# Performance work log

Hardware: AMD Instinct MI355X
Metric: run time of the kernel (lower is better)

Reference implementation:

```python
import jax, jax.numpy as jnp
import numpy as np


def _lga_pass(x, filters, radius):
    # x: [N, C, H, W]; filters: [N, (2r+1)^2, H, W]
    # out[n,c,h,w] = sum_{i,j in [-r,r]} filters[n,(i+r)*(2r+1)+(j+r),h,w] * x[n,c,h+i,w+j]
    N, C, H, W = x.shape
    k = 2 * radius + 1
    xp = jnp.pad(x, ((0, 0), (0, 0), (radius, radius), (radius, radius)))
    out = jnp.zeros_like(x)
    idx = 0
    for i in range(k):  # fixed small kernel loop (25 taps), accumulates without materializing [N,C,H,W,25]
        for j in range(k):
            out = out + filters[:, idx:idx + 1] * xp[:, :, i:i + H, j:j + W]
            idx += 1
    return out


def setup_inputs() -> dict:
    key = jax.random.key(0)
    k1, k2 = jax.random.split(key)
    input1 = jax.random.normal(k1, (2, 64, 256, 512), dtype=jnp.float32)
    input2 = jax.random.uniform(k2, (2, 25, 256, 512), dtype=jnp.float32)
    return {"input1": input1, "input2": input2, "radius": 2}


def reference(input1, input2, radius):
    # LGA applied twice with the same per-pixel filters (Lga2Function.forward)
    temp = _lga_pass(input1, input2, radius)
    out = _lga_pass(temp, input2, radius)
    return out
```

## Files before the change

kernel.cpp:

```cpp
#include <hip/hip_runtime.h>
#include <hip/hip_fp16.h>


typedef __fp16 h2v __attribute__((ext_vector_type(2)));

#define OH 12
#define OW 60
#define USH 40

__device__ __forceinline__ unsigned pkh(float a, float b) {
    union { h2v h; unsigned u; } c;
    c.h = __builtin_amdgcn_cvt_pkrtz(a, b);
    return c.u;
}

#define PKF(ac, fv, xv) \
    asm("v_pk_fma_f16 %0, %1, %2, %0" : "+v"(ac) : "v"(fv), "v"(xv));

#define ROWP(i, w0, w1, w2, w3, D01, D23) { \
    const unsigned A01 = ((w0) >> 16) | ((w1) << 16); \
    const unsigned A12 = ((w1) >> 16) | ((w2) << 16); \
    const unsigned A23 = ((w2) >> 16) | ((w3) << 16); \
    PKF(D01, frA[5*(i)+0], w0)  PKF(D01, frA[5*(i)+1], A01) \
    PKF(D01, frA[5*(i)+2], w1)  PKF(D01, frA[5*(i)+3], A12) \
    PKF(D01, frA[5*(i)+4], w2) \
    PKF(D23, frB[5*(i)+0], w1)  PKF(D23, frB[5*(i)+1], A12) \
    PKF(D23, frB[5*(i)+2], w2)  PKF(D23, frB[5*(i)+3], A23) \
    PKF(D23, frB[5*(i)+4], w3) }

#define PASSP(BUF, ROWBASE) { \
    unsigned e01 = 0u, o01 = 0u, e23 = 0u, o23 = 0u; \
    _Pragma("unroll") \
    for (int i = 0; i < 5; ++i) { \
        const int b = ((ROWBASE) + i) * USH + 2 * s; \
        uint2 lo = *(const uint2*)&(BUF)[b]; \
        uint2 hi = *(const uint2*)&(BUF)[b + 2]; \
        if (i & 1) { ROWP(i, lo.x, lo.y, hi.x, hi.y, o01, o23) } \
        else       { ROWP(i, lo.x, lo.y, hi.x, hi.y, e01, e23) } \
    } \
    asm("v_pk_add_f16 %0, %1, %2" : "=v"(s01) : "v"(e01), "v"(o01)); \
    asm("v_pk_add_f16 %0, %1, %2" : "=v"(s23) : "v"(e23), "v"(o23)); }

#define LBAR() { asm volatile("s_waitcnt lgkmcnt(0)" ::: "memory"); \
                 __builtin_amdgcn_s_barrier(); asm volatile("" ::: "memory"); }

__global__ __launch_bounds__(256)
void lga2_fused(const float* __restrict__ x, const float* __restrict__ f,
                float* __restrict__ out, int N, int C, int H, int W, int CPB) {
    const int tid = threadIdx.x;
    const int r = tid >> 4;
    const int s = tid & 15;
    const int oh0 = blockIdx.y * OH;
    const int ow0 = blockIdx.x * OW;
    const int CG = C / CPB;
    const int n  = blockIdx.z / CG;
    const int c0 = (blockIdx.z % CG) * CPB;
    const int HW = H * W;

    __shared__ unsigned sxU[2][20 * USH];
    __shared__ unsigned stU[16 * USH];

    if (tid < 32) {
        int row = tid & 15;
        stU[row * USH + ((tid & 16) ? 33 : 0)] = 0u;
    }

    const int gh_f = oh0 - 2 + r;
    const int gwb  = ow0 - 2 + 4 * s;
    const bool rowok = (gh_f >= 0) && (gh_f < H);
    const bool p0ok = rowok && (gwb >= 0) && (gwb + 1 < W);
    const bool p1ok = rowok && (gwb + 3 < W);
    const float* fb = f + (size_t)(n * 25) * HW + (size_t)(rowok ? gh_f : 0) * W;

    unsigned frA[25], frB[25];
    #pragma unroll
    for (int t = 0; t < 25; ++t) {
        float2 v01 = p0ok ? *(const float2*)(fb + (size_t)t * HW + gwb)
                          : make_float2(0.f, 0.f);
        float2 v23 = p1ok ? *(const float2*)(fb + (size_t)t * HW + gwb + 2)
                          : make_float2(0.f, 0.f);
        frA[t] = pkh(v01.x, v01.y);
        frB[t] = pkh(v23.x, v23.y);
        if (t == 12) __builtin_amdgcn_sched_barrier(0);
    }
    #pragma unroll
    for (int t = 0; t < 25; ++t)
        asm volatile("" : "+v"(frA[t]), "+v"(frB[t]));

    const int i1 = tid + 256;
    const bool has1 = (tid < 340 - 256);
    const int row0 = tid / 17, v0 = tid - row0 * 17;
    const int row1 = i1 / 17,  v1 = i1 - row1 * 17;
    const int g0h = oh0 - 4 + row0, g0c = ow0 - 4 + 4 * v0;
    const int g1h = oh0 - 4 + row1, g1c = ow0 - 4 + 4 * v1;
    const bool ok0 = (g0h >= 0) && (g0h < H) && (g0c >= 0) && (g0c + 3 < W);
    const bool ok1 = has1 && (g1h >= 0) && (g1h < H) && (g1c >= 0) && (g1c + 3 < W);
    const int off0 = ok0 ? (g0h * W + g0c) : 0;
    const int off1 = ok1 ? (g1h * W + g1c) : 0;
    const int l0u = row0 * USH + 2 * v0;
    const int l1u = row1 * USH + 2 * v1;

    const float4 z4 = make_float4(0.f, 0.f, 0.f, 0.f);
    const float* xc = x + (size_t)(n * C + c0) * HW;

    {
        float4 p = ok0 ? *(const float4*)(xc + off0) : z4;
        *(uint2*)&sxU[0][l0u] = make_uint2(pkh(p.x, p.y), pkh(p.z, p.w));
        if (has1) {
            float4 q = ok1 ? *(const float4*)(xc + off1) : z4;
            *(uint2*)&sxU[0][l1u] = make_uint2(pkh(q.x, q.y), pkh(q.z, q.w));
        }
    }
    __syncthreads();

    const bool prow = (r >= 2) && (r <= 13) && (gh_f < H);
    const int rc = (r < 2) ? 2 : ((r > 13) ? 13 : r);
    float* op = out + ((size_t)(n * C + c0) * H + gh_f) * W + gwb;

    int cur = 0;
    for (int cc = 0; cc < CPB; ++cc) {
        float4 nx0 = z4, nx1 = z4;
        const bool pf = (cc + 1 < CPB);
        if (pf) {
            const float* xn = xc + (size_t)(cc + 1) * HW;
            if (ok0) nx0 = *(const float4*)(xn + off0);
            if (ok1) nx1 = *(const float4*)(xn + off1);
        }

        unsigned s01, s23;
        PASSP(sxU[cur], r)
        stU[r * USH + 1 + 2 * s] = s01;
        stU[r * USH + 2 + 2 * s] = s23;
        LBAR();

        PASSP(stU, rc - 2)
        if (prow) {
            union { unsigned u; h2v h; } U01, U23;
            U01.u = s01; U23.u = s23;
            if (s >= 1 && gwb + 1 < W)
                *(float2*)op = make_float2((float)U01.h.x, (float)U01.h.y);
            if (s <= 14 && gwb + 3 < W)
                *(float2*)(op + 2) = make_float2((float)U23.h.x, (float)U23.h.y);
        }

        if (pf) {
            *(uint2*)&sxU[cur ^ 1][l0u] = make_uint2(pkh(nx0.x, nx0.y), pkh(nx0.z, nx0.w));
            if (has1)
                *(uint2*)&sxU[cur ^ 1][l1u] = make_uint2(pkh(nx1.x, nx1.y), pkh(nx1.z, nx1.w));
        }
        LBAR();
        cur ^= 1;
        op += HW;
    }
}

extern "C" void kernel_launch(void* const* d_in, const int* in_sizes, int n_in,
                              void* d_out, int out_size, void* d_ws, size_t ws_size,
                              hipStream_t stream) {
    const float* x = (const float*)d_in[0];
    const float* f = (const float*)d_in[1];
    float* out = (float*)d_out;

    const int N = 2, C = 64, H = 256, W = 512;
    const int CPB = 32;
    const int CG = C / CPB;

    dim3 grid((W + OW - 1) / OW,
              (H + OH - 1) / OH,
              N * CG);
    lga2_fused<<<grid, 256, 0, stream>>>(x, f, out, N, C, H, W, CPB);
}
```

Baseline: 74.27 us.

## Pack two channels per half2 lane to process channel pairs per iteration

Changes the shared-memory layout so each packed fp16 word holds the same pixel from two adjacent channels rather than two adjacent pixels. The inner FMA uses op_sel to broadcast a single filter half across both lanes, which removes the shift/or work that built misaligned pixel pairs and halves the number of barrier-separated iterations. In exchange it uses wider LDS rows, 128-bit LDS loads, more accumulator registers, and twice the global loads and stores per iteration, which may raise register pressure.

```diff
diff --git a/kernel.cpp b/kernel.cpp
--- a/kernel.cpp
+++ b/kernel.cpp
@@ -6,7 +6,7 @@
 
 #define OH 12
 #define OW 60
-#define USH 40
+#define USH 76
 
 __device__ __forceinline__ unsigned pkh(float a, float b) {
     union { h2v h; unsigned u; } c;
@@ -14,32 +14,34 @@
     return c.u;
 }
 
-#define PKF(ac, fv, xv) \
-    asm("v_pk_fma_f16 %0, %1, %2, %0" : "+v"(ac) : "v"(fv), "v"(xv));
+#define PKFL(ac, fv, xv) \
+    asm("v_pk_fma_f16 %0, %1, %2, %0 op_sel:[0,0,0] op_sel_hi:[0,1,1]" \
+        : "+v"(ac) : "v"(fv), "v"(xv));
+#define PKFH(ac, fv, xv) \
+    asm("v_pk_fma_f16 %0, %1, %2, %0 op_sel:[1,0,0] op_sel_hi:[1,1,1]" \
+        : "+v"(ac) : "v"(fv), "v"(xv));
 
-#define ROWP(i, w0, w1, w2, w3, D01, D23) { \
-    const unsigned A01 = ((w0) >> 16) | ((w1) << 16); \
-    const unsigned A12 = ((w1) >> 16) | ((w2) << 16); \
-    const unsigned A23 = ((w2) >> 16) | ((w3) << 16); \
-    PKF(D01, frA[5*(i)+0], w0)  PKF(D01, frA[5*(i)+1], A01) \
-    PKF(D01, frA[5*(i)+2], w1)  PKF(D01, frA[5*(i)+3], A12) \
-    PKF(D01, frA[5*(i)+4], w2) \
-    PKF(D23, frB[5*(i)+0], w1)  PKF(D23, frB[5*(i)+1], A12) \
-    PKF(D23, frB[5*(i)+2], w2)  PKF(D23, frB[5*(i)+3], A23) \
-    PKF(D23, frB[5*(i)+4], w3) }
+#define ROW8(T, qa, qb, A0, A1, A2, A3) \
+  PKFL(A0, frA[T+0], qa.x) PKFH(A1, frA[T+0], qa.y) PKFL(A2, frB[T+0], qa.z) PKFH(A3, frB[T+0], qa.w) \
+  PKFL(A0, frA[T+1], qa.y) PKFH(A1, frA[T+1], qa.z) PKFL(A2, frB[T+1], qa.w) PKFH(A3, frB[T+1], qb.x) \
+  PKFL(A0, frA[T+2], qa.z) PKFH(A1, frA[T+2], qa.w) PKFL(A2, frB[T+2], qb.x) PKFH(A3, frB[T+2], qb.y) \
+  PKFL(A0, frA[T+3], qa.w) PKFH(A1, frA[T+3], qb.x) PKFL(A2, frB[T+3], qb.y) PKFH(A3, frB[T+3], qb.z) \
+  PKFL(A0, frA[T+4], qb.x) PKFH(A1, frA[T+4], qb.y) PKFL(A2, frB[T+4], qb.z) PKFH(A3, frB[T+4], qb.w)
 
-#define PASSP(BUF, ROWBASE) { \
-    unsigned e01 = 0u, o01 = 0u, e23 = 0u, o23 = 0u; \
+#define PASS2(BUF, ROWBASE, S0, S1, S2, S3) { \
+    unsigned e0=0u,e1=0u,e2=0u,e3=0u,o0=0u,o1=0u,o2=0u,o3=0u; \
     _Pragma("unroll") \
     for (int i = 0; i < 5; ++i) { \
-        const int b = ((ROWBASE) + i) * USH + 2 * s; \
-        uint2 lo = *(const uint2*)&(BUF)[b]; \
-        uint2 hi = *(const uint2*)&(BUF)[b + 2]; \
-        if (i & 1) { ROWP(i, lo.x, lo.y, hi.x, hi.y, o01, o23) } \
-        else       { ROWP(i, lo.x, lo.y, hi.x, hi.y, e01, e23) } \
+        const int b = ((ROWBASE) + i) * USH + 4 * s; \
+        uint4 qa = *(const uint4*)&(BUF)[b]; \
+        uint4 qb = *(const uint4*)&(BUF)[b + 4]; \
+        if (i & 1) { ROW8(5*i, qa, qb, o0, o1, o2, o3) } \
+        else       { ROW8(5*i, qa, qb, e0, e1, e2, e3) } \
     } \
-    asm("v_pk_add_f16 %0, %1, %2" : "=v"(s01) : "v"(e01), "v"(o01)); \
-    asm("v_pk_add_f16 %0, %1, %2" : "=v"(s23) : "v"(e23), "v"(o23)); }
+    asm("v_pk_add_f16 %0, %1, %2" : "=v"(S0) : "v"(e0), "v"(o0)); \
+    asm("v_pk_add_f16 %0, %1, %2" : "=v"(S1) : "v"(e1), "v"(o1)); \
+    asm("v_pk_add_f16 %0, %1, %2" : "=v"(S2) : "v"(e2), "v"(o2)); \
+    asm("v_pk_add_f16 %0, %1, %2" : "=v"(S3) : "v"(e3), "v"(o3)); }
 
 #define LBAR() { asm volatile("s_waitcnt lgkmcnt(0)" ::: "memory"); \
                  __builtin_amdgcn_s_barrier(); asm volatile("" ::: "memory"); }
@@ -60,9 +62,9 @@
     __shared__ unsigned sxU[2][20 * USH];
     __shared__ unsigned stU[16 * USH];
 
-    if (tid < 32) {
-        int row = tid & 15;
-        stU[row * USH + ((tid & 16) ? 33 : 0)] = 0u;
+    if (tid < 64) {
+        int row = tid >> 2, q = tid & 3;
+        stU[row * USH + (q < 2 ? q : q + 64)] = 0u;
     }
 
     const int gh_f = oh0 - 2 + r;
@@ -97,18 +99,23 @@
     const bool ok1 = has1 && (g1h >= 0) && (g1h < H) && (g1c >= 0) && (g1c + 3 < W);
     const int off0 = ok0 ? (g0h * W + g0c) : 0;
     const int off1 = ok1 ? (g1h * W + g1c) : 0;
-    const int l0u = row0 * USH + 2 * v0;
-    const int l1u = row1 * USH + 2 * v1;
+    const int l0u = row0 * USH + 4 * v0;
+    const int l1u = row1 * USH + 4 * v1;
 
     const float4 z4 = make_float4(0.f, 0.f, 0.f, 0.f);
     const float* xc = x + (size_t)(n * C + c0) * HW;
 
+#define PACK4(pa, pb) make_uint4(pkh(pa.x, pb.x), pkh(pa.y, pb.y), \
+                                 pkh(pa.z, pb.z), pkh(pa.w, pb.w))
+
     {
-        float4 p = ok0 ? *(const float4*)(xc + off0) : z4;
-        *(uint2*)&sxU[0][l0u] = make_uint2(pkh(p.x, p.y), pkh(p.z, p.w));
+        float4 pa = ok0 ? *(const float4*)(xc + off0) : z4;
+        float4 pb = ok0 ? *(const float4*)(xc + HW + off0) : z4;
+        *(uint4*)&sxU[0][l0u] = PACK4(pa, pb);
         if (has1) {
-            float4 q = ok1 ? *(const float4*)(xc + off1) : z4;
-            *(uint2*)&sxU[0][l1u] = make_uint2(pkh(q.x, q.y), pkh(q.z, q.w));
+            float4 qa = ok1 ? *(const float4*)(xc + off1) : z4;
+            float4 qb = ok1 ? *(const float4*)(xc + HW + off1) : z4;
+            *(uint4*)&sxU[0][l1u] = PACK4(qa, qb);
         }
     }
     __syncthreads();
@@ -118,39 +125,46 @@
     float* op = out + ((size_t)(n * C + c0) * H + gh_f) * W + gwb;
 
     int cur = 0;
-    for (int cc = 0; cc < CPB; ++cc) {
-        float4 nx0 = z4, nx1 = z4;
-        const bool pf = (cc + 1 < CPB);
+    for (int cp = 0; cp < CPB; cp += 2) {
+        float4 n0a = z4, n0b = z4, n1a = z4, n1b = z4;
+        const bool pf = (cp + 2 < CPB);
         if (pf) {
-            const float* xn = xc + (size_t)(cc + 1) * HW;
-            if (ok0) nx0 = *(const float4*)(xn + off0);
-            if (ok1) nx1 = *(const float4*)(xn + off1);
+            const float* xn = xc + (size_t)(cp + 2) * HW;
+            if (ok0) { n0a = *(const float4*)(xn + off0);
+                       n0b = *(const float4*)(xn + HW + off0); }
+            if (ok1) { n1a = *(const float4*)(xn + off1);
+                       n1b = *(const float4*)(xn + HW + off1); }
         }
 
-        unsigned s01, s23;
-        PASSP(sxU[cur], r)
-        stU[r * USH + 1 + 2 * s] = s01;
-        stU[r * USH + 2 + 2 * s] = s23;
+        unsigned t0, t1, t2, t3;
+        PASS2(sxU[cur], r, t0, t1, t2, t3)
+        *(uint2*)&stU[r * USH + 2 + 4 * s] = make_uint2(t0, t1);
+        *(uint2*)&stU[r * USH + 4 + 4 * s] = make_uint2(t2, t3);
         LBAR();
 
-        PASSP(stU, rc - 2)
+        PASS2(stU, rc - 2, t0, t1, t2, t3)
         if (prow) {
-            union { unsigned u; h2v h; } U01, U23;
-            U01.u = s01; U23.u = s23;
-            if (s >= 1 && gwb + 1 < W)
-                *(float2*)op = make_float2((float)U01.h.x, (float)U01.h.y);
-            if (s <= 14 && gwb + 3 < W)
-                *(float2*)(op + 2) = make_float2((float)U23.h.x, (float)U23.h.y);
+            union { unsigned u; h2v h; } U0, U1, U2, U3;
+            U0.u = t0; U1.u = t1; U2.u = t2; U3.u = t3;
+            float* oq = op + HW;
+            if (s >= 1 && gwb + 1 < W) {
+                *(float2*)op = make_float2((float)U0.h.x, (float)U1.h.x);
+                *(float2*)oq = make_float2((float)U0.h.y, (float)U1.h.y);
+            }
+            if (s <= 14 && gwb + 3 < W) {
+                *(float2*)(op + 2) = make_float2((float)U2.h.x, (float)U3.h.x);
+                *(float2*)(oq + 2) = make_float2((float)U2.h.y, (float)U3.h.y);
+            }
         }
 
         if (pf) {
-            *(uint2*)&sxU[cur ^ 1][l0u] = make_uint2(pkh(nx0.x, nx0.y), pkh(nx0.z, nx0.w));
-            if (has1)
-                *(uint2*)&sxU[cur ^ 1][l1u] = make_uint2(pkh(nx1.x, nx1.y), pkh(nx1.z, nx1.w));
+            unsigned* d = sxU[cur ^ 1];
+            *(uint4*)&d[l0u] = PACK4(n0a, n0b);
+            if (has1) *(uint4*)&d[l1u] = PACK4(n1a, n1b);
         }
         LBAR();
         cur ^= 1;
-        op += HW;
+        op += 2 * (size_t)HW;
     }
 }
 
```

Result: faster. 69.67 us (-6.2%).
